# Optimization experiments

Hardware: AMD Instinct MI355X
Metric: run time of the kernel (lower is better)

Reference implementation:

```python
import jax, jax.numpy as jnp
import numpy as np

H = 32      # query heads
HK = 8      # kv heads
HD = 64     # head dim
D = 2048    # model dim
BASE = 10000.0
NEG = -1e9


def _rope_cos_sin(L):
    inv_freq = 1.0 / (BASE ** (jnp.arange(0, HD, 2, dtype=jnp.float32) / HD))  # [HD/2]
    freqs = jnp.arange(L, dtype=jnp.float32)[:, None] * inv_freq[None, :]       # [L, HD/2]
    emb = jnp.concatenate([freqs, freqs], axis=-1)                               # [L, HD]
    return jnp.cos(emb), jnp.sin(emb)


def _rotate_half(x):
    x1, x2 = jnp.split(x, 2, axis=-1)
    return jnp.concatenate([-x2, x1], axis=-1)


def setup_inputs() -> dict:
    key = jax.random.key(0)
    ks = jax.random.split(key, 5)
    B, L = 2, 2048
    x = jax.random.normal(ks[0], (B, L, D), dtype=jnp.float32)
    Wq = jax.random.normal(ks[1], (D, D), dtype=jnp.float32) * 0.02
    Wk = jax.random.normal(ks[2], (HK * HD, D), dtype=jnp.float32) * 0.02
    Wv = jax.random.normal(ks[3], (HK * HD, D), dtype=jnp.float32) * 0.02
    Wo = jax.random.normal(ks[4], (D, D), dtype=jnp.float32) * 0.02
    causal = jnp.where(jnp.tril(jnp.ones((L, L), dtype=bool)), 0.0, NEG)
    mask = causal[None, None].astype(jnp.float32)  # [1,1,L,L] additive mask
    return {"x": x, "Wq": Wq, "Wk": Wk, "Wv": Wv, "Wo": Wo, "mask": mask}


def reference(x, Wq, Wk, Wv, Wo, mask):
    B, L, _ = x.shape
    # projections (nn.Linear: y = x @ W^T), split heads -> [B, heads, L, HD]
    q = jnp.einsum('bld,ed->ble', x, Wq).reshape(B, L, H, HD).transpose(0, 2, 1, 3)
    k = jnp.einsum('bld,ed->ble', x, Wk).reshape(B, L, HK, HD).transpose(0, 2, 1, 3)
    v = jnp.einsum('bld,ed->ble', x, Wv).reshape(B, L, HK, HD).transpose(0, 2, 1, 3)
    # RoPE (plain branch: L <= original_max); cos/sin [L,HD] broadcast over B,heads
    cos, sin = _rope_cos_sin(L)
    q = q * cos + _rotate_half(q) * sin
    k = k * cos + _rotate_half(k) * sin
    # GQA: repeat_interleave kv heads to H heads
    rep = H // HK
    k = jnp.repeat(k, rep, axis=1)  # [B,H,L,HD]
    v = jnp.repeat(v, rep, axis=1)
    scores = jnp.einsum('bhld,bhmd->bhlm', q, k) / np.float32(np.sqrt(HD)) + mask
    attn = jax.nn.softmax(scores, axis=-1)
    out = jnp.einsum('bhlm,bhmd->blhd', attn, v).reshape(B, L, D)
    return jnp.einsum('ble,de->bld', out, Wo)
```

## Files before the change

kernel.cpp:

```cpp
#include <hip/hip_runtime.h>
#include <math.h>

#define NH 32
#define NHK 8
#define HD 64
#define DMODEL 2048
#define LSEQ 2048
#define NB 2
#define QKV_N 3072

typedef __attribute__((ext_vector_type(8))) short short8;
typedef __attribute__((ext_vector_type(4))) float floatx4;

__device__ __forceinline__ unsigned short f2bf(float f) {
  unsigned u = __float_as_uint(f);
  return (unsigned short)((u + 0x7FFFu + ((u >> 16) & 1u)) >> 16);
}
__device__ __forceinline__ float bf2f(unsigned short v) {
  return __uint_as_float((unsigned)v << 16);
}
__device__ __forceinline__ float fast_exp2(float x) {
#if __has_builtin(__builtin_amdgcn_exp2f)
  return __builtin_amdgcn_exp2f(x);
#else
  return __expf(x * 0.69314718f);
#endif
}
__device__ __forceinline__ unsigned pack_bf_trunc(float hi, float lo) {
  return __builtin_amdgcn_perm(__float_as_uint(hi), __float_as_uint(lo), 0x07060302u);
}
__device__ __forceinline__ void stage16(const unsigned short* g,
                                        unsigned short* lds_wave_base, int lane) {
#if __has_builtin(__builtin_amdgcn_global_load_lds)
  __builtin_amdgcn_global_load_lds(
      (const __attribute__((address_space(1))) void*)(g),
      (__attribute__((address_space(3))) void*)(lds_wave_base), 16, 0, 0);
#else
  *(uint4*)(lds_wave_base + lane * 8) = *(const uint4*)g;
#endif
}
__device__ __forceinline__ void stage16g(const char* g_lane,
                                         unsigned short* lds_wave_base, int lane) {
#if __has_builtin(__builtin_amdgcn_global_load_lds)
  __builtin_amdgcn_global_load_lds(
      (const __attribute__((address_space(1))) void*)(g_lane),
      (__attribute__((address_space(3))) void*)(lds_wave_base), 16, 0, 0);
#else
  *(uint4*)(lds_wave_base + lane * 8) = *(const uint4*)g_lane;
#endif
}

__global__ __launch_bounds__(256) void rope_tab(float2* __restrict__ tab) {
  int i = blockIdx.x * 256 + threadIdx.x;
  int d = i & 31, l = i >> 5;
  float invf = (float)pow(10000.0, -(double)d / 32.0);
  float ang = (float)l * invf;
  double sd, cd;
  sincos((double)ang, &sd, &cd);
  tab[i] = make_float2((float)cd, (float)sd);
}

__global__ __launch_bounds__(256) void cvt_bf16(const float* __restrict__ src,
                                                unsigned short* __restrict__ dst,
                                                int n4) {
  int i = blockIdx.x * 256 + threadIdx.x;
  if (i >= n4) return;
  float4 v = ((const float4*)src)[i];
  ushort4 o;
  o.x = f2bf(v.x); o.y = f2bf(v.y); o.z = f2bf(v.z); o.w = f2bf(v.w);
  ((ushort4*)dst)[i] = o;
}

__global__ __launch_bounds__(256) void cvt_w3(const float* __restrict__ Wq,
                                              const float* __restrict__ Wk,
                                              const float* __restrict__ Wv,
                                              unsigned short* __restrict__ dst) {
  const int NQ = DMODEL * DMODEL / 4, NK = 512 * DMODEL / 4;
  int i = blockIdx.x * 256 + threadIdx.x;
  const float* src;
  int off;
  if (i < NQ) { src = Wq; off = i; }
  else if (i < NQ + NK) { src = Wk; off = i - NQ; }
  else { src = Wv; off = i - NQ - NK; }
  float4 v = ((const float4*)src)[off];
  ushort4 o;
  o.x = f2bf(v.x); o.y = f2bf(v.y); o.z = f2bf(v.z); o.w = f2bf(v.w);
  ((ushort4*)dst)[i] = o;
}

template <bool BF16C>
__global__ __launch_bounds__(256) void gemm2(const unsigned short* __restrict__ A,
                                             const unsigned short* __restrict__ B,
                                             void* __restrict__ Cv, int K, int ldc) {
  __shared__ unsigned short As[128 * 32];
  __shared__ unsigned short Bs[128 * 32];
  const int tid = threadIdx.x;
  const int wave = tid >> 6, lane = tid & 63;
  const int quad = lane >> 4, l16 = lane & 15;
  const int m0 = blockIdx.y * 128, n0 = blockIdx.x * 128;
  const int wm = (wave & 1) * 64, wn = (wave >> 1) * 64;

  const int srow = wave * 16 + (lane >> 2);
  const int schunk = (lane & 3) ^ ((lane >> 2) & 3);
  const unsigned short* Asrc = A + (size_t)(m0 + srow) * K + schunk * 8;
  const unsigned short* Bsrc = B + (size_t)(n0 + srow) * K + schunk * 8;
  unsigned short* AdstL = &As[wave * 512];
  unsigned short* AdstH = &As[2048 + wave * 512];
  unsigned short* BdstL = &Bs[wave * 512];
  unsigned short* BdstH = &Bs[2048 + wave * 512];
  const size_t rstep = (size_t)64 * K;

  const int sw = (quad ^ (l16 & 3)) * 8;
  floatx4 acc[4][4] = {};

  for (int k0 = 0; k0 < K; k0 += 32) {
    __syncthreads();
    stage16(Asrc + k0, AdstL, lane);
    stage16(Asrc + rstep + k0, AdstH, lane);
    stage16(Bsrc + k0, BdstL, lane);
    stage16(Bsrc + rstep + k0, BdstH, lane);
    __syncthreads();
    short8 af[4], bfr[4];
#pragma unroll
    for (int i = 0; i < 4; ++i)
      af[i] = *(const short8*)&As[(wm + i * 16 + l16) * 32 + sw];
#pragma unroll
    for (int j = 0; j < 4; ++j)
      bfr[j] = *(const short8*)&Bs[(wn + j * 16 + l16) * 32 + sw];
#pragma unroll
    for (int i = 0; i < 4; ++i)
#pragma unroll
      for (int j = 0; j < 4; ++j)
        acc[i][j] = __builtin_amdgcn_mfma_f32_16x16x32_bf16(af[i], bfr[j], acc[i][j], 0, 0, 0);
  }

#pragma unroll
  for (int i = 0; i < 4; ++i)
#pragma unroll
    for (int j = 0; j < 4; ++j)
#pragma unroll
      for (int r = 0; r < 4; ++r) {
        size_t idx = (size_t)(m0 + wm + i * 16 + quad * 4 + r) * ldc + n0 + wn + j * 16 + l16;
        if (BF16C)
          ((unsigned short*)Cv)[idx] = f2bf(acc[i][j][r]);
        else
          ((float*)Cv)[idx] = acc[i][j][r];
      }
}

__global__ __launch_bounds__(256) void ropek_cvt2(const unsigned short* __restrict__ qkvb,
                                                  const float2* __restrict__ tab,
                                                  unsigned short* __restrict__ kb) {
  int t = blockIdx.x * 256 + threadIdx.x;
  int d = t & 31;
  int rest = t >> 5;
  int khead = rest & 7;
  int bl = rest >> 3;
  int l = bl & (LSEQ - 1);
  int b = bl >> 11;
  const unsigned short* src = qkvb + (size_t)bl * QKV_N + DMODEL + khead * HD;
  float2 cs = tab[(size_t)l * 32 + d];
  float x1 = bf2f(src[d]), x2 = bf2f(src[d + 32]);
  unsigned short* dst = kb + ((size_t)((b * NHK + khead) * LSEQ + l)) * HD;
  dst[d] = f2bf(x1 * cs.x - x2 * cs.y);
  dst[d + 32] = f2bf(x2 * cs.x + x1 * cs.y);
}

__global__ __launch_bounds__(256) void vt_cvt2(const unsigned short* __restrict__ qkvb,
                                               unsigned short* __restrict__ vtb) {
  __shared__ unsigned short Lt[64][72];
  const int tt = blockIdx.x, kh = blockIdx.y, b = blockIdx.z;
  const int tid = threadIdx.x;
  const unsigned short* src =
      qkvb + ((size_t)(b * LSEQ + tt * 64)) * QKV_N + DMODEL + 512 + kh * HD;
  {
    int row = tid >> 2, c0 = (tid & 3) * 16;
    *(uint4*)&Lt[row][c0] = *(const uint4*)(src + (size_t)row * QKV_N + c0);
    *(uint4*)&Lt[row][c0 + 8] = *(const uint4*)(src + (size_t)row * QKV_N + c0 + 8);
  }
  __syncthreads();
  {
    int d = tid >> 2, seg = tid & 3;
    unsigned short o[16];
#pragma unroll
    for (int k = 0; k < 16; ++k) o[k] = Lt[seg * 16 + k][d];
    unsigned short* dst =
        vtb + ((size_t)((b * NHK + kh) * 80 + d)) * LSEQ + tt * 64 + seg * 16;
    *(uint4*)dst = *(uint4*)o;
    *(uint4*)(dst + 8) = *(uint4*)(o + 8);
  }
  if (tid < 64)
    vtb[((size_t)((b * NHK + kh) * 80 + 64)) * LSEQ + tt * 64 + tid] = 0x3F80;
}

__global__ __launch_bounds__(256, 2) void attn8(const unsigned short* __restrict__ qkvb,
                                                const float2* __restrict__ tab,
                                                const unsigned short* __restrict__ kb,
                                                const unsigned short* __restrict__ vtb,
                                                unsigned short* __restrict__ out) {
  const int kh = blockIdx.x;
  const int p = blockIdx.y;
  const int b = blockIdx.z;
  const int wave = threadIdx.x >> 6, lane = threadIdx.x & 63;
  const int quad = lane >> 4, l16 = lane & 15;
  const int h = kh * 4 + wave;

  __shared__ unsigned short Kbuf[2][64 * 64];
  __shared__ unsigned short Vbuf[2][80 * 64];
  __shared__ unsigned short Ps_all[4][32][72];
  unsigned short(*Ps)[72] = Ps_all[wave];

  const char* kbaseB = (const char*)(kb + ((size_t)(b * NHK + kh) * LSEQ) * HD);
  const char* vbaseB = (const char*)(vtb + ((size_t)(b * NHK + kh) * 80) * LSEQ);
  const float QSCALE = 0.125f * 1.44269504f;

  short8 qf[2][2];
  floatx4 O[2][5];

  auto loadQ = [&](int qb) {
#pragma unroll
    for (int i = 0; i < 2; ++i) {
      const int tok = qb + i * 16 + l16;
      const unsigned short* qr =
          qkvb + ((size_t)(b * LSEQ + tok)) * QKV_N + h * HD + quad * 8;
      uint4 lo = *(const uint4*)qr;
      uint4 hi = *(const uint4*)(qr + 32);
      const float2* tr = tab + (size_t)tok * 32 + quad * 8;
      float4 cs01 = ((const float4*)tr)[0];
      float4 cs23 = ((const float4*)tr)[1];
      float4 cs45 = ((const float4*)tr)[2];
      float4 cs67 = ((const float4*)tr)[3];
      float cosv[8] = {cs01.x, cs01.z, cs23.x, cs23.z, cs45.x, cs45.z, cs67.x, cs67.z};
      float sinv[8] = {cs01.y, cs01.w, cs23.y, cs23.w, cs45.y, cs45.w, cs67.y, cs67.w};
      const unsigned short* plo = (const unsigned short*)&lo;
      const unsigned short* phi = (const unsigned short*)&hi;
      unsigned short olo[8], ohi[8];
#pragma unroll
      for (int j = 0; j < 8; ++j) {
        float x1 = bf2f(plo[j]), x2 = bf2f(phi[j]);
        olo[j] = f2bf((x1 * cosv[j] - x2 * sinv[j]) * QSCALE);
        ohi[j] = f2bf((x2 * cosv[j] + x1 * sinv[j]) * QSCALE);
      }
      qf[i][0] = *(const short8*)olo;
      qf[i][1] = *(const short8*)ohi;
    }
  };
  auto zeroO = [&]() {
#pragma unroll
    for (int i = 0; i < 2; ++i)
#pragma unroll
      for (int j = 0; j < 5; ++j) O[i][j] = (floatx4){0.f, 0.f, 0.f, 0.f};
  };
  auto epilogue = [&](int qb) {
#pragma unroll
    for (int i = 0; i < 2; ++i) {
      float lv = __shfl(O[i][4][0], l16);
      float inv = 1.0f / lv;
      const size_t obase =
          ((size_t)(b * LSEQ + qb + i * 16 + l16)) * DMODEL + h * HD;
#pragma unroll
      for (int j = 0; j < 4; ++j) {
        uint2 w;
        w.x = (unsigned)f2bf(O[i][j][0] * inv) | ((unsigned)f2bf(O[i][j][1] * inv) << 16);
        w.y = (unsigned)f2bf(O[i][j][2] * inv) | ((unsigned)f2bf(O[i][j][3] * inv) << 16);
        *(uint2*)&out[obase + j * 16 + quad * 4] = w;
      }
    }
  };
  auto stageKV = [&](int bi, int kt) {
    unsigned short* Kd = Kbuf[bi];
    unsigned short* Vd = Vbuf[bi];
#pragma unroll
    for (int c = wave; c < 18; c += 4) {
      if (c < 8) {
        int o = c * 1024 + lane * 16;
        int row = o >> 7;
        int lgc = ((o >> 4) & 7) ^ (row & 7);
        stage16g(kbaseB + (size_t)(kt * 64 + row) * 128 + lgc * 16,
                 Kd + c * 512, lane);
      } else {
        int o = (c - 8) * 1024 + lane * 16;
        int row = o >> 7;
        int lgc = ((o >> 4) & 7) ^ (row & 7);
        stage16g(vbaseB + (size_t)row * (LSEQ * 2) + (size_t)kt * 128 + lgc * 16,
                 Vd + (c - 8) * 512, lane);
      }
    }
  };

  const int last0 = p >> 1;
  const int last1 = (63 - p) >> 1;
  const int qb0 = p * 32, qb1 = (63 - p) * 32;
  const int N = last0 + last1 + 2;

  loadQ(qb0);
  zeroO();
  stageKV(0, 0);
  int qb = qb0, lastk = last0;

#pragma unroll 1
  for (int m = 0; m < N; ++m) {
    __syncthreads();

    if (m + 1 < N) {
      int kt2 = (m + 1 > last0) ? (m - last0) : (m + 1);
      stageKV((m + 1) & 1, kt2);
    }
    if (m == last0 + 1) {
      epilogue(qb0);
      zeroO();
      loadQ(qb1);
      qb = qb1;
      lastk = last1;
    }

    const int kt = (m > last0) ? (m - last0 - 1) : m;
    const unsigned short* Ks = Kbuf[m & 1];
    const unsigned short* Vs = Vbuf[m & 1];

    short8 kf[4][2];
#pragma unroll
    for (int t = 0; t < 4; ++t)
#pragma unroll
      for (int hf = 0; hf < 2; ++hf) {
        int row = t * 16 + l16;
        int phys = (4 * hf + quad) ^ (row & 7);
        kf[t][hf] = *(const short8*)&Ks[row * 64 + phys * 8];
      }

    floatx4 st[4][2];
#pragma unroll
    for (int t = 0; t < 4; ++t)
#pragma unroll
      for (int i = 0; i < 2; ++i) {
        floatx4 z = {0.f, 0.f, 0.f, 0.f};
        z = __builtin_amdgcn_mfma_f32_16x16x32_bf16(kf[t][0], qf[i][0], z, 0, 0, 0);
        st[t][i] = __builtin_amdgcn_mfma_f32_16x16x32_bf16(kf[t][1], qf[i][1], z, 0, 0, 0);
      }

    if (kt == lastk) {
      const int kofs = kt * 64 - qb;
#pragma unroll
      for (int t = 0; t < 4; ++t) {
        const int krow = kofs + 16 * t + quad * 4;
#pragma unroll
        for (int i = 0; i < 2; ++i) {
          const int qcol = 16 * i + l16;
          float sv[4];
#pragma unroll
          for (int r = 0; r < 4; ++r) {
            float v = st[t][i][r];
            if (krow + r > qcol) v = -1e30f;
            sv[r] = fast_exp2(v);
          }
          uint2 w;
          w.x = pack_bf_trunc(sv[1], sv[0]);
          w.y = pack_bf_trunc(sv[3], sv[2]);
          *(uint2*)&Ps[16 * i + l16][16 * t + quad * 4] = w;
        }
      }
    } else {
#pragma unroll
      for (int t = 0; t < 4; ++t)
#pragma unroll
        for (int i = 0; i < 2; ++i) {
          float sv[4];
#pragma unroll
          for (int r = 0; r < 4; ++r) sv[r] = fast_exp2(st[t][i][r]);
          uint2 w;
          w.x = pack_bf_trunc(sv[1], sv[0]);
          w.y = pack_bf_trunc(sv[3], sv[2]);
          *(uint2*)&Ps[16 * i + l16][16 * t + quad * 4] = w;
        }
    }

    short8 pf[2][2];
#pragma unroll
    for (int i = 0; i < 2; ++i)
#pragma unroll
      for (int hh = 0; hh < 2; ++hh)
        pf[i][hh] = *(const short8*)&Ps[16 * i + l16][32 * hh + quad * 8];
#pragma unroll
    for (int j = 0; j < 5; ++j) {
      int row = j * 16 + l16;
      short8 vf0 = *(const short8*)&Vs[row * 64 + ((quad ^ (row & 7)) * 8)];
      short8 vf1 = *(const short8*)&Vs[row * 64 + (((4 + quad) ^ (row & 7)) * 8)];
#pragma unroll
      for (int i = 0; i < 2; ++i) {
        O[i][j] = __builtin_amdgcn_mfma_f32_16x16x32_bf16(vf0, pf[i][0], O[i][j], 0, 0, 0);
        O[i][j] = __builtin_amdgcn_mfma_f32_16x16x32_bf16(vf1, pf[i][1], O[i][j], 0, 0, 0);
      }
    }
  }

  epilogue(qb1);
}

extern "C" void kernel_launch(void* const* d_in, const int* in_sizes, int n_in,
                              void* d_out, int out_size, void* d_ws,
                              size_t ws_size, hipStream_t stream) {
  const float* x = (const float*)d_in[0];
  const float* Wq = (const float*)d_in[1];
  const float* Wk = (const float*)d_in[2];
  const float* Wv = (const float*)d_in[3];
  const float* Wo = (const float*)d_in[4];
  float* out = (float*)d_out;

  char* ws = (char*)d_ws;
  unsigned short* qkvb = (unsigned short*)ws;
  float2* tab = (float2*)(ws + 25165824);
  unsigned short* kbuf = (unsigned short*)(ws + 25690112);
  unsigned short* vtb = (unsigned short*)(ws + 29884416);
  unsigned short* xb = (unsigned short*)(ws + 35127296);
  unsigned short* wqkvb = (unsigned short*)(ws + 51904512);
  unsigned short* aob = xb;
  unsigned short* wob = wqkvb;

  const int M = NB * LSEQ;
  dim3 blk(256);

  rope_tab<<<(LSEQ * 32) / 256, blk, 0, stream>>>(tab);
  cvt_bf16<<<(M * DMODEL / 4 + 255) / 256, blk, 0, stream>>>(x, xb, M * DMODEL / 4);
  cvt_w3<<<(QKV_N * DMODEL / 4) / 256, blk, 0, stream>>>(Wq, Wk, Wv, wqkvb);

  gemm2<true><<<dim3(QKV_N / 128, M / 128), blk, 0, stream>>>(xb, wqkvb, qkvb, DMODEL, QKV_N);

  ropek_cvt2<<<(NB * LSEQ * 8 * 32) / 256, blk, 0, stream>>>(qkvb, tab, kbuf);
  vt_cvt2<<<dim3(LSEQ / 64, NHK, NB), blk, 0, stream>>>(qkvb, vtb);

  attn8<<<dim3(NHK, 32, NB), blk, 0, stream>>>(qkvb, tab, kbuf, vtb, aob);

  cvt_bf16<<<(DMODEL * DMODEL / 4 + 255) / 256, blk, 0, stream>>>(Wo, wob, DMODEL * DMODEL / 4);

  gemm2<false><<<dim3(DMODEL / 128, M / 128), blk, 0, stream>>>(aob, wob, out, DMODEL, DMODEL);
}
```

Baseline: 319.6 us.

## Replace GEMM with 512-thread 4-stage pipelined kernel with larger tiles

Replaces the single-buffered 128x128 GEMM with a 512-thread kernel using 256xBN tiles and a four-deep LDS ring. Loads are issued three tiles ahead with explicit vmcnt waits and raw barriers, and each tile's MFMA work is split into two halves interleaved with the next stage's loads. It also sets wave priority around MFMA bursts. The aim is to hide global-load latency and raise data reuse in both projection GEMMs, in exchange for much more LDS and register pressure and hand-tuned waitcnt counts that must match the number of loads issued.

```diff
diff --git a/kernel.cpp b/kernel.cpp
--- a/kernel.cpp
+++ b/kernel.cpp
@@ -28,16 +28,6 @@
 }
 __device__ __forceinline__ unsigned pack_bf_trunc(float hi, float lo) {
   return __builtin_amdgcn_perm(__float_as_uint(hi), __float_as_uint(lo), 0x07060302u);
-}
-__device__ __forceinline__ void stage16(const unsigned short* g,
-                                        unsigned short* lds_wave_base, int lane) {
-#if __has_builtin(__builtin_amdgcn_global_load_lds)
-  __builtin_amdgcn_global_load_lds(
-      (const __attribute__((address_space(1))) void*)(g),
-      (__attribute__((address_space(3))) void*)(lds_wave_base), 16, 0, 0);
-#else
-  *(uint4*)(lds_wave_base + lane * 8) = *(const uint4*)g;
-#endif
 }
 __device__ __forceinline__ void stage16g(const char* g_lane,
                                          unsigned short* lds_wave_base, int lane) {
@@ -88,59 +78,105 @@
   ((ushort4*)dst)[i] = o;
 }
 
-template <bool BF16C>
-__global__ __launch_bounds__(256) void gemm2(const unsigned short* __restrict__ A,
-                                             const unsigned short* __restrict__ B,
-                                             void* __restrict__ Cv, int K, int ldc) {
-  __shared__ unsigned short As[128 * 32];
-  __shared__ unsigned short Bs[128 * 32];
+template <int BN, bool BF16C>
+__global__ __launch_bounds__(512, 2) void gemm8(const unsigned short* __restrict__ A,
+                                                const unsigned short* __restrict__ B,
+                                                void* __restrict__ Cv, int K, int ldc) {
+  constexpr int CN = BN / 64;
+  constexpr int BUFB = BN * 32;
+  __shared__ unsigned short As[4 * 256 * 32];
+  __shared__ unsigned short Bs[4 * BUFB];
+
   const int tid = threadIdx.x;
   const int wave = tid >> 6, lane = tid & 63;
   const int quad = lane >> 4, l16 = lane & 15;
-  const int m0 = blockIdx.y * 128, n0 = blockIdx.x * 128;
-  const int wm = (wave & 1) * 64, wn = (wave >> 1) * 64;
-
-  const int srow = wave * 16 + (lane >> 2);
-  const int schunk = (lane & 3) ^ ((lane >> 2) & 3);
-  const unsigned short* Asrc = A + (size_t)(m0 + srow) * K + schunk * 8;
-  const unsigned short* Bsrc = B + (size_t)(n0 + srow) * K + schunk * 8;
-  unsigned short* AdstL = &As[wave * 512];
-  unsigned short* AdstH = &As[2048 + wave * 512];
-  unsigned short* BdstL = &Bs[wave * 512];
-  unsigned short* BdstH = &Bs[2048 + wave * 512];
-  const size_t rstep = (size_t)64 * K;
-
-  const int sw = (quad ^ (l16 & 3)) * 8;
-  floatx4 acc[4][4] = {};
-
-  for (int k0 = 0; k0 < K; k0 += 32) {
-    __syncthreads();
-    stage16(Asrc + k0, AdstL, lane);
-    stage16(Asrc + rstep + k0, AdstH, lane);
-    stage16(Bsrc + k0, BdstL, lane);
-    stage16(Bsrc + rstep + k0, BdstH, lane);
-    __syncthreads();
-    short8 af[4], bfr[4];
+  const int wm = wave & 1, wn = wave >> 1;
+  const int m0 = blockIdx.y * 256, n0 = blockIdx.x * BN;
+  const int kt = K >> 5;
+
+  const int sgrow = wave * 16 + (lane >> 2);
+  const int cchunk = (lane & 3) ^ ((lane >> 3) & 3);
+  const char* AgB = (const char*)(A + (size_t)(m0 + sgrow) * K + cchunk * 8);
+  const char* BgB = (const char*)(B + (size_t)(n0 + sgrow) * K + cchunk * 8);
+
+  auto stageA = [&](int t2) {
+    unsigned short* dst = &As[((t2 & 3) << 13) + wave * 512];
+#pragma unroll
+    for (int u = 0; u < 2; ++u)
+      stage16g(AgB + ((size_t)u * 128 * K + (size_t)t2 * 32) * 2, dst + u * 4096, lane);
+  };
+  auto stageB = [&](int t2) {
+    unsigned short* dst = &Bs[(t2 & 3) * BUFB + wave * 512];
+#pragma unroll
+    for (int u = 0; u < BN / 128; ++u)
+      stage16g(BgB + ((size_t)u * 128 * K + (size_t)t2 * 32) * 2, dst + u * 4096, lane);
+  };
+
+  const int sw8 = (quad ^ ((l16 >> 1) & 3)) * 8;
+
+  floatx4 acc[8][CN] = {};
+
+  stageA(0); stageB(0);
+  stageA(1); stageB(1);
+  stageA(2); stageB(2);
+
+#pragma unroll 1
+  for (int t = 0; t < kt; ++t) {
+    if (t + 2 < kt) {
+      if constexpr (BN == 256) asm volatile("s_waitcnt vmcnt(8)" ::: "memory");
+      else                     asm volatile("s_waitcnt vmcnt(6)" ::: "memory");
+    } else if (t + 1 < kt) {
+      if constexpr (BN == 256) asm volatile("s_waitcnt vmcnt(4)" ::: "memory");
+      else                     asm volatile("s_waitcnt vmcnt(3)" ::: "memory");
+    } else {
+      asm volatile("s_waitcnt vmcnt(0)" ::: "memory");
+    }
+    __builtin_amdgcn_s_barrier();
+    __builtin_amdgcn_sched_barrier(0);
+
+    const unsigned short* Asb = &As[(t & 3) << 13];
+    const unsigned short* Bsb = &Bs[(t & 3) * BUFB];
+    const unsigned short* Arow = Asb + (wm * 128 + l16) * 32 + sw8;
+    const unsigned short* Brow = Bsb + (wn * 16 * CN + l16) * 32 + sw8;
+
+    short8 bfr[CN], af[4];
+#pragma unroll
+    for (int j = 0; j < CN; ++j) bfr[j] = *(const short8*)(Brow + j * 16 * 32);
+#pragma unroll
+    for (int i = 0; i < 4; ++i) af[i] = *(const short8*)(Arow + i * 16 * 32);
+
+    if (t + 3 < kt) stageA(t + 3);
+
+    __builtin_amdgcn_s_setprio(1);
 #pragma unroll
     for (int i = 0; i < 4; ++i)
-      af[i] = *(const short8*)&As[(wm + i * 16 + l16) * 32 + sw];
-#pragma unroll
-    for (int j = 0; j < 4; ++j)
-      bfr[j] = *(const short8*)&Bs[(wn + j * 16 + l16) * 32 + sw];
+#pragma unroll
+      for (int j = 0; j < CN; ++j)
+        acc[i][j] = __builtin_amdgcn_mfma_f32_16x16x32_bf16(af[i], bfr[j], acc[i][j], 0, 0, 0);
+    __builtin_amdgcn_s_setprio(0);
+
+#pragma unroll
+    for (int i = 0; i < 4; ++i) af[i] = *(const short8*)(Arow + (64 + i * 16) * 32);
+
+    if (t + 3 < kt) stageB(t + 3);
+
+    __builtin_amdgcn_s_setprio(1);
 #pragma unroll
     for (int i = 0; i < 4; ++i)
 #pragma unroll
-      for (int j = 0; j < 4; ++j)
-        acc[i][j] = __builtin_amdgcn_mfma_f32_16x16x32_bf16(af[i], bfr[j], acc[i][j], 0, 0, 0);
+      for (int j = 0; j < CN; ++j)
+        acc[4 + i][j] = __builtin_amdgcn_mfma_f32_16x16x32_bf16(af[i], bfr[j], acc[4 + i][j], 0, 0, 0);
+    __builtin_amdgcn_s_setprio(0);
   }
 
 #pragma unroll
-  for (int i = 0; i < 4; ++i)
-#pragma unroll
-    for (int j = 0; j < 4; ++j)
+  for (int i = 0; i < 8; ++i)
+#pragma unroll
+    for (int j = 0; j < CN; ++j)
 #pragma unroll
       for (int r = 0; r < 4; ++r) {
-        size_t idx = (size_t)(m0 + wm + i * 16 + quad * 4 + r) * ldc + n0 + wn + j * 16 + l16;
+        size_t idx = (size_t)(m0 + wm * 128 + i * 16 + quad * 4 + r) * ldc +
+                     n0 + wn * 16 * CN + j * 16 + l16;
         if (BF16C)
           ((unsigned short*)Cv)[idx] = f2bf(acc[i][j][r]);
         else
@@ -423,7 +459,8 @@
   cvt_bf16<<<(M * DMODEL / 4 + 255) / 256, blk, 0, stream>>>(x, xb, M * DMODEL / 4);
   cvt_w3<<<(QKV_N * DMODEL / 4) / 256, blk, 0, stream>>>(Wq, Wk, Wv, wqkvb);
 
-  gemm2<true><<<dim3(QKV_N / 128, M / 128), blk, 0, stream>>>(xb, wqkvb, qkvb, DMODEL, QKV_N);
+  gemm8<256, true><<<dim3(QKV_N / 256, M / 256), dim3(512), 0, stream>>>(
+      xb, wqkvb, qkvb, DMODEL, QKV_N);
 
   ropek_cvt2<<<(NB * LSEQ * 8 * 32) / 256, blk, 0, stream>>>(qkvb, tab, kbuf);
   vt_cvt2<<<dim3(LSEQ / 64, NHK, NB), blk, 0, stream>>>(qkvb, vtb);
@@ -432,5 +469,6 @@
 
   cvt_bf16<<<(DMODEL * DMODEL / 4 + 255) / 256, blk, 0, stream>>>(Wo, wob, DMODEL * DMODEL / 4);
 
-  gemm2<false><<<dim3(DMODEL / 128, M / 128), blk, 0, stream>>>(aob, wob, out, DMODEL, DMODEL);
-}
+  gemm8<128, false><<<dim3(DMODEL / 128, M / 256), dim3(512), 0, stream>>>(
+      aob, wob, out, DMODEL, DMODEL);
+}
```

Result: faster. 302.9 us (-5.2%).
